# Kernel tuning notes

Hardware: AMD Instinct MI355X
Metric: run time of the kernel (lower is better)

Reference implementation:

```python
import jax, jax.numpy as jnp
import numpy as np

B, C, H, W = 4, 256, 128, 128
SP, HEADS = 4, 2
SCALE = (C // HEADS) ** -0.5  # module uses full dim//num_heads, not per-branch head dim
EPS = 1e-4
CB = C // 2  # channels per strip branch


def setup_inputs() -> dict:
    key = jax.random.key(0)
    ks = jax.random.split(key, 8)
    return {
        "x": jax.random.normal(ks[0], (B, C, H, W), jnp.float32),
        "ln_g": jnp.ones((C,), jnp.float32),
        "ln_b": jnp.zeros((C,), jnp.float32),
        "w_qkv": jax.random.normal(ks[1], (C, 3 * C), jnp.float32) * 0.02,
        "lepe_w1": jax.random.normal(ks[2], (CB, 1, 3, 3), jnp.float32) * 0.1,
        "lepe_b1": jnp.zeros((CB,), jnp.float32),
        "lepe_w2": jax.random.normal(ks[3], (CB, 1, 3, 3), jnp.float32) * 0.1,
        "lepe_b2": jnp.zeros((CB,), jnp.float32),
        "proj_w": jax.random.normal(ks[4], (C, C), jnp.float32) * 0.02,
        "proj_b": jnp.zeros((C,), jnp.float32),
    }


def _strip_branch(q, k, v, h, hsp, w, wsp, lepe_w, lepe_b):
    # q,k,v: [B, L=h*hsp*w*wsp, CB]; channel layout is (c head) -> head fastest
    cd = CB // HEADS
    nwin = B * h * w

    def to_win(t):  # -> [(b h w), head, hsp*wsp, cd]
        t = t.reshape(B, h, hsp, w, wsp, cd, HEADS)
        t = t.transpose(0, 1, 3, 6, 2, 4, 5)  # B,h,w,head,hsp,wsp,cd
        return t.reshape(nwin, HEADS, hsp * wsp, cd)

    qw, kw, vw = to_win(q), to_win(k), to_win(v)

    # LePE: depthwise 3x3 conv on v laid out as [(b h w), (c head), hsp, wsp]
    vim = vw.reshape(nwin, HEADS, hsp, wsp, cd).transpose(0, 4, 1, 2, 3)
    vim = vim.reshape(nwin, CB, hsp, wsp)
    lepe = jax.lax.conv_general_dilated(vim, lepe_w, (1, 1), 'SAME',
                                        feature_group_count=CB)
    lepe = lepe + lepe_b[None, :, None, None]
    lepe = lepe.reshape(nwin, cd, HEADS, hsp, wsp).transpose(0, 2, 3, 4, 1)
    lepe = lepe.reshape(nwin, HEADS, hsp * wsp, cd)

    attn = jax.nn.softmax(jnp.einsum('whqc,whkc->whqk', qw * SCALE, kw), axis=-1)
    o = jnp.einsum('whqk,whkc->whqc', attn, vw) + lepe
    # back to b (c head) (h hsp) (w wsp)
    o = o.reshape(B, h, w, HEADS, hsp, wsp, cd)
    o = o.transpose(0, 6, 3, 1, 4, 2, 5).reshape(B, CB, h * hsp, w * wsp)
    return o


def reference(x, ln_g, ln_b, w_qkv, lepe_w1, lepe_b1, lepe_w2, lepe_b2, proj_w, proj_b):
    # tokens [B, H*W, C]
    xp = x.transpose(0, 2, 3, 1).reshape(B, H * W, C)
    mu = xp.mean(-1, keepdims=True)
    var = ((xp - mu) ** 2).mean(-1, keepdims=True)
    xp = (xp - mu) * jax.lax.rsqrt(var + EPS) * ln_g + ln_b

    qkv = xp @ w_qkv
    q, k, v = jnp.split(qkv, 3, axis=-1)

    # branch 1: horizontal strips (h=1, hsp=H, w=W/SP, wsp=SP) on first channel half
    x1 = _strip_branch(q[..., :CB], k[..., :CB], v[..., :CB],
                       1, H, W // SP, SP, lepe_w1, lepe_b1)
    # branch 2: vertical strips (h=H/SP, hsp=SP, w=1, wsp=W) on second half
    x2 = _strip_branch(q[..., CB:], k[..., CB:], v[..., CB:],
                       H // SP, SP, 1, W, lepe_w2, lepe_b2)

    xc = jnp.concatenate([x1, x2], axis=1)  # [B, C, H, W]
    out = jnp.einsum('bchw,oc->bohw', xc, proj_w) + proj_b[None, :, None, None]
    return out
```

## Files before the change

### kernel.cpp

```cpp
#include <hip/hip_runtime.h>
#include <stdint.h>

#define T_ 65536
#define HW_ 16384
#define SCALE_F 0.08838834764831845f
#define EPS_ 1e-4f

typedef unsigned short u16;
typedef unsigned int u32;
typedef __attribute__((ext_vector_type(4))) float f32x4;
typedef __attribute__((ext_vector_type(8))) __bf16 bf16x8v;

union frag_u { u16 h[8]; bf16x8v v; uint4 q4; };

__device__ __forceinline__ float bf2f(u16 h) {
    union { u32 u; float f; } x; x.u = ((u32)h) << 16; return x.f;
}
__device__ __forceinline__ u16 f2bf(float f) {
    union { u32 u; float f; } x; x.f = f;
    u32 u = x.u;
    return (u16)((u + 0x7FFFu + ((u >> 16) & 1u)) >> 16);
}
__device__ __forceinline__ f32x4 mfma_b(bf16x8v a, bf16x8v b, f32x4 c) {
    return __builtin_amdgcn_mfma_f32_16x16x32_bf16(a, b, c, 0, 0, 0);
}
__device__ __forceinline__ void gl_lds16(const u16* g, u16* l) {
    __builtin_amdgcn_global_load_lds(
        (const __attribute__((address_space(1))) void*)g,
        (__attribute__((address_space(3))) void*)l, 16, 0, 0);
}

__device__ __forceinline__ int u2t(int u, int br) {
    if (br == 1) return u;
    int b = u >> 14, rr = u & 16383;
    int s = rr >> 9, rem = rr & 511;
    int y = rem >> 2, xl = rem & 3;
    return (b << 14) + (y << 7) + (s << 2) + xl;
}
__device__ __forceinline__ int t2u0(int t) {
    int b = t >> 14, rr = t & 16383;
    int y = rr >> 7, x = rr & 127;
    return (b << 14) + ((x >> 2) << 9) + (y << 2) + (x & 3);
}

__global__ void sentinel_kernel(float* out, float code) {
    if (blockIdx.x == 0 && threadIdx.x == 0) out[0] = code;
}

__global__ __launch_bounds__(256) void wconv_kernel(const float* __restrict__ w,
        const float* __restrict__ pw, u16* __restrict__ wt, u16* __restrict__ pwc) {
    __shared__ float lds[64 * 65];
    int bid = blockIdx.x;
    int tid = threadIdx.x;
    if (bid < 48) {
        int c0 = (bid % 12) * 64, k0 = (bid / 12) * 64;
        for (int i = 0; i < 16; ++i) {
            int e = i * 256 + tid;
            int k = e >> 6, c = e & 63;
            lds[k * 65 + c] = w[(size_t)(k0 + k) * 768 + c0 + c];
        }
        __syncthreads();
        for (int i = 0; i < 16; ++i) {
            int e = i * 256 + tid;
            int c = e >> 6, k = e & 63;
            wt[(size_t)(c0 + c) * 256 + k0 + k] = f2bf(lds[k * 65 + c]);
        }
    } else {
        int base = (bid - 48) * 2048;
        for (int i = 0; i < 8; ++i) {
            int e = base + i * 256 + tid;
            int m = e >> 8, ks = e & 255;
            int c = (ks < 128) ? (2 * (ks & 63) + (ks >> 6))
                               : (128 + 2 * ((ks - 128) & 63) + ((ks - 128) >> 6));
            pwc[e] = f2bf(pw[(size_t)m * 256 + c]);
        }
    }
}

__global__ __launch_bounds__(512, 2) void ln_kernel(const float* __restrict__ x,
        const float* __restrict__ g, const float* __restrict__ bta, u16* __restrict__ xn) {
    __shared__ float reds[8][260];
    __shared__ float redss[8][260];
    __shared__ float mus[256];
    __shared__ float rstds[256];
    int tid = threadIdx.x, lane = tid & 63, w = tid >> 6;
    int w32 = w * 32;
    int tok0 = blockIdx.x * 256 + lane * 4;
    int b = tok0 >> 14, hw = tok0 & 16383;
    const float* xb = x + (size_t)b * 256 * HW_ + hw;
    float4 v[32];
    #pragma unroll
    for (int j = 0; j < 32; ++j)
        v[j] = *(const float4*)(xb + (size_t)(w32 + j) * HW_);
    float s0 = 0.f, s1 = 0.f, s2 = 0.f, s3 = 0.f;
    float q0 = 0.f, q1 = 0.f, q2 = 0.f, q3 = 0.f;
    #pragma unroll
    for (int j = 0; j < 32; ++j) {
        s0 += v[j].x; q0 += v[j].x * v[j].x;
        s1 += v[j].y; q1 += v[j].y * v[j].y;
        s2 += v[j].z; q2 += v[j].z * v[j].z;
        s3 += v[j].w; q3 += v[j].w * v[j].w;
    }
    *(float4*)&reds[w][lane * 4]  = make_float4(s0, s1, s2, s3);
    *(float4*)&redss[w][lane * 4] = make_float4(q0, q1, q2, q3);
    __syncthreads();
    if (tid < 256) {
        float S = 0.f, SS = 0.f;
        #pragma unroll
        for (int p = 0; p < 8; ++p) { S += reds[p][tid]; SS += redss[p][tid]; }
        float mu = S * (1.f / 256.f);
        float var = SS * (1.f / 256.f) - mu * mu;
        mus[tid] = mu;
        rstds[tid] = rsqrtf(var + EPS_);
    }
    __syncthreads();
    float4 mu4 = *(const float4*)&mus[lane * 4];
    float4 rs4 = *(const float4*)&rstds[lane * 4];
    float mk[4] = {mu4.x, mu4.y, mu4.z, mu4.w};
    float rk[4] = {rs4.x, rs4.y, rs4.z, rs4.w};
    #pragma unroll
    for (int k = 0; k < 4; ++k) {
        u16 tmp[32] __attribute__((aligned(16)));
        #pragma unroll
        for (int j = 0; j < 32; ++j) {
            int c = w32 + j;
            float xv = (k == 0) ? v[j].x : (k == 1) ? v[j].y : (k == 2) ? v[j].z : v[j].w;
            tmp[j] = f2bf((xv - mk[k]) * rk[k] * g[c] + bta[c]);
        }
        u16* o = xn + (size_t)(tok0 + k) * 256 + w32;
        *(uint4*)(o)      = *(const uint4*)&tmp[0];
        *(uint4*)(o + 8)  = *(const uint4*)&tmp[8];
        *(uint4*)(o + 16) = *(const uint4*)&tmp[16];
        *(uint4*)(o + 24) = *(const uint4*)&tmp[24];
    }
}

__global__ __launch_bounds__(256) void qkv_gemm(const u16* __restrict__ wt,
        const u16* __restrict__ xn, u16* __restrict__ qkt, u16* __restrict__ vpl, int br) {
    __shared__ __align__(16) u16 a_tile[2][128 * 32];
    __shared__ __align__(16) u16 b_tile[2][128 * 32];
    int my = blockIdx.y;
    int n0 = blockIdx.x * 128;
    int tid = threadIdx.x;
    int lane = tid & 63, wid = tid >> 6;
    int wm = wid >> 1, wn = wid & 1;
    int l15 = lane & 15, quad = lane >> 4;
    int colbase = (my == 0) ? (br * 128) : (my == 1 ? (256 + br * 128) : (512 + br * 128));
    int srow = tid >> 2, sgg = tid & 3;
    const u16* gA0 = wt + (size_t)(colbase + srow) * 256 + sgg * 8;
    const u16* gA1 = gA0 + (size_t)64 * 256;
    const u16* gB0 = xn + (size_t)u2t(n0 + srow, br) * 256 + sgg * 8;
    const u16* gB1 = xn + (size_t)u2t(n0 + srow + 64, br) * 256 + sgg * 8;
    int lb0 = wid * 1024, lb1 = 4096 + wid * 1024;
    gl_lds16(gA0, (u16*)((char*)&a_tile[0][0] + lb0));
    gl_lds16(gA1, (u16*)((char*)&a_tile[0][0] + lb1));
    gl_lds16(gB0, (u16*)((char*)&b_tile[0][0] + lb0));
    gl_lds16(gB1, (u16*)((char*)&b_tile[0][0] + lb1));
    f32x4 acc[4][4] = {};
    for (int ks = 0; ks < 8; ++ks) {
        __syncthreads();
        int cur = ks & 1;
        if (ks < 7) {
            int k0 = (ks + 1) * 32;
            int nb = cur ^ 1;
            gl_lds16(gA0 + k0, (u16*)((char*)&a_tile[nb][0] + lb0));
            gl_lds16(gA1 + k0, (u16*)((char*)&a_tile[nb][0] + lb1));
            gl_lds16(gB0 + k0, (u16*)((char*)&b_tile[nb][0] + lb0));
            gl_lds16(gB1 + k0, (u16*)((char*)&b_tile[nb][0] + lb1));
        }
        bf16x8v af[4], bf[4];
        #pragma unroll
        for (int i = 0; i < 4; ++i) {
            af[i] = *(const bf16x8v*)&a_tile[cur][(wm * 64 + i * 16 + l15) * 32 + quad * 8];
            bf[i] = *(const bf16x8v*)&b_tile[cur][(wn * 64 + i * 16 + l15) * 32 + quad * 8];
        }
        #pragma unroll
        for (int i = 0; i < 4; ++i)
            #pragma unroll
            for (int j = 0; j < 4; ++j)
                acc[i][j] = mfma_b(af[i], bf[j], acc[i][j]);
    }
    if (my < 2) {
        int cb2 = my * 128;
        #pragma unroll
        for (int i = 0; i < 4; ++i) {
            #pragma unroll
            for (int r = 0; r < 4; ++r) {
                int cl = wm * 64 + i * 16 + quad * 4 + r;
                int col = cb2 + ((cl & 1) << 6) + (cl >> 1);
                #pragma unroll
                for (int j = 0; j < 4; ++j) {
                    int u = n0 + wn * 64 + j * 16 + l15;
                    qkt[(size_t)u * 256 + col] = f2bf(acc[i][j][r]);
                }
            }
        }
    } else {
        #pragma unroll
        for (int i = 0; i < 4; ++i) {
            int pbase = wm * 64 + i * 16 + quad * 4;
            #pragma unroll
            for (int j = 0; j < 4; ++j) {
                int u = n0 + wn * 64 + j * 16 + l15;
                #pragma unroll
                for (int r = 0; r < 4; ++r)
                    vpl[(size_t)(pbase + r) * T_ + u] = f2bf(acc[i][j][r]);
            }
        }
    }
}

__global__ __launch_bounds__(512, 4) void attn_kernel(const u16* __restrict__ qkt,
        const u16* __restrict__ vpl, u16* __restrict__ xcb, int stride) {
    __shared__ __align__(16) u16 k_area[2][128 * 72];
    __shared__ __align__(16) u16 v_lds[2][64 * 136];
    int bid = blockIdx.x;
    int id2 = (bid & 7) * 128 + (bid >> 3);
    int window = id2 >> 3, h = (id2 >> 2) & 1, qq = id2 & 3;
    int wbase = window * 512;
    int tid = threadIdx.x, lane = tid & 63, wid = tid >> 6;
    int l15 = lane & 15, quad = lane >> 4;

    frag_u af[2];
    {
        size_t qrow = (size_t)(wbase + qq * 128 + wid * 16 + l15) * 256 + h * 64 + quad * 8;
        af[0].q4 = *(const uint4*)&qkt[qrow];
        af[1].q4 = *(const uint4*)&qkt[qrow + 32];
    }
    for (int idx = tid; idx < 1024; idx += 512) {
        int tok = idx >> 3, c8 = (idx & 7) * 8;
        *(uint4*)&k_area[0][tok * 72 + c8] =
            *(const uint4*)&qkt[(size_t)(wbase + tok) * 256 + 128 + h * 64 + c8];
    }
    for (int idx = tid; idx < 1024; idx += 512) {
        int cd = idx >> 4, k8 = (idx & 15) * 8;
        *(uint4*)&v_lds[0][cd * 136 + k8] =
            *(const uint4*)&vpl[(size_t)(2 * cd + h) * T_ + wbase + k8];
    }
    __syncthreads();

    float m[4] = {-1e30f, -1e30f, -1e30f, -1e30f};
    float l[4] = {0.f, 0.f, 0.f, 0.f};
    f32x4 acc_o[4] = {};
    for (int ch = 0; ch < 4; ++ch) {
        int cur = ch & 1, nxt = cur ^ 1;
        if (ch < 3) {
            for (int idx = tid; idx < 1024; idx += 512) {
                int tok = idx >> 3, c8 = (idx & 7) * 8;
                *(uint4*)&k_area[nxt][tok * 72 + c8] =
                    *(const uint4*)&qkt[(size_t)(wbase + (ch + 1) * 128 + tok) * 256 + 128 + h * 64 + c8];
            }
            for (int idx = tid; idx < 1024; idx += 512) {
                int cd = idx >> 4, k8 = (idx & 15) * 8;
                *(uint4*)&v_lds[nxt][cd * 136 + k8] =
                    *(const uint4*)&vpl[(size_t)(2 * cd + h) * T_ + wbase + (ch + 1) * 128 + k8];
            }
        }
        f32x4 s[8];
        #pragma unroll
        for (int kt = 0; kt < 8; ++kt) {
            f32x4 z = {0.f, 0.f, 0.f, 0.f};
            bf16x8v b0 = *(const bf16x8v*)&k_area[cur][(kt * 16 + l15) * 72 + quad * 8];
            bf16x8v b1 = *(const bf16x8v*)&k_area[cur][(kt * 16 + l15) * 72 + 32 + quad * 8];
            z = mfma_b(af[0].v, b0, z);
            z = mfma_b(af[1].v, b1, z);
            s[kt] = z;
        }
        float cmx[4] = {-1e30f, -1e30f, -1e30f, -1e30f};
        #pragma unroll
        for (int kt = 0; kt < 8; ++kt)
            #pragma unroll
            for (int r = 0; r < 4; ++r) cmx[r] = fmaxf(cmx[r], s[kt][r]);
        #pragma unroll
        for (int d = 1; d < 16; d <<= 1)
            #pragma unroll
            for (int r = 0; r < 4; ++r) cmx[r] = fmaxf(cmx[r], __shfl_xor(cmx[r], d, 16));
        float alpha[4];
        #pragma unroll
        for (int r = 0; r < 4; ++r) {
            float mn = fmaxf(m[r], cmx[r]);
            alpha[r] = __expf((m[r] - mn) * SCALE_F);
            m[r] = mn;
        }
        float ps[4] = {0.f, 0.f, 0.f, 0.f};
        #pragma unroll
        for (int kt = 0; kt < 8; ++kt)
            #pragma unroll
            for (int r = 0; r < 4; ++r) {
                float p = __expf((s[kt][r] - m[r]) * SCALE_F);
                s[kt][r] = p;
                ps[r] += p;
            }
        #pragma unroll
        for (int r = 0; r < 4; ++r) l[r] = l[r] * alpha[r] + ps[r];
        #pragma unroll
        for (int cs = 0; cs < 4; ++cs)
            #pragma unroll
            for (int r = 0; r < 4; ++r) acc_o[cs][r] *= alpha[r];
        __syncthreads();
        u16* p_lds = &k_area[cur][wid * 1152];
        #pragma unroll
        for (int half = 0; half < 2; ++half) {
            #pragma unroll
            for (int kt4 = 0; kt4 < 4; ++kt4)
                #pragma unroll
                for (int rr = 0; rr < 4; ++rr)
                    p_lds[(quad * 4 + rr) * 72 + kt4 * 16 + l15] = f2bf(s[half * 4 + kt4][rr]);
            #pragma unroll
            for (int k32 = 0; k32 < 2; ++k32) {
                bf16x8v pa = *(const bf16x8v*)&p_lds[l15 * 72 + k32 * 32 + quad * 8];
                #pragma unroll
                for (int cs = 0; cs < 4; ++cs) {
                    bf16x8v vf = *(const bf16x8v*)&v_lds[cur]
                        [(cs * 16 + l15) * 136 + half * 64 + k32 * 32 + quad * 8];
                    acc_o[cs] = mfma_b(pa, vf, acc_o[cs]);
                }
            }
        }
        __syncthreads();
    }
    float linv[4];
    #pragma unroll
    for (int r = 0; r < 4; ++r) {
        float v = l[r];
        #pragma unroll
        for (int d = 1; d < 16; d <<= 1) v += __shfl_xor(v, d, 16);
        linv[r] = 1.f / v;
    }
    #pragma unroll
    for (int cs = 0; cs < 4; ++cs) {
        int col = h * 64 + cs * 16 + l15;
        #pragma unroll
        for (int r = 0; r < 4; ++r) {
            int u = wbase + qq * 128 + wid * 16 + quad * 4 + r;
            xcb[(size_t)u * stride + col] = f2bf(acc_o[cs][r] * linv[r]);
        }
    }
}

__global__ __launch_bounds__(512) void lepe_kernel(const u16* __restrict__ vpl,
        const float* __restrict__ lw, const float* __restrict__ lb,
        u16* __restrict__ xcb, int stride, int br) {
    __shared__ __align__(16) u16 o_s[512 * 72];
    int hh = blockIdx.x & 1, wdw = blockIdx.x >> 1;
    int wbase = wdw * 512;
    int tid = threadIdx.x;
    int xd = (br == 0) ? 4 : 128;
    for (int i = 0; i < 8; ++i) {
        int g = i * 512 + tid;
        int cd = g >> 6, u0 = (g & 63) * 8;
        int cl = 2 * cd + hh;
        const u16* vp = vpl + (size_t)cl * T_ + wbase;
        const float* wp = lw + cl * 9;
        float bias = lb[cl];
        float acc[8];
        #pragma unroll
        for (int j = 0; j < 8; ++j) acc[j] = bias;
        #pragma unroll
        for (int r = -1; r <= 1; ++r) {
            int offA = u0 + r * xd;
            int offB = offA + 4;
            float m[8];
            if (offA >= 0 && offA <= 508) {
                uint2 va = *(const uint2*)&vp[offA];
                u16 ha[4]; *(uint2*)ha = va;
                #pragma unroll
                for (int j = 0; j < 4; ++j) m[j] = bf2f(ha[j]);
            } else { m[0] = m[1] = m[2] = m[3] = 0.f; }
            if (offB >= 0 && offB <= 508) {
                uint2 vb = *(const uint2*)&vp[offB];
                u16 hb[4]; *(uint2*)hb = vb;
                #pragma unroll
                for (int j = 0; j < 4; ++j) m[4 + j] = bf2f(hb[j]);
            } else { m[4] = m[5] = m[6] = m[7] = 0.f; }
            float le = 0.f, re = 0.f;
            if (br == 1) {
                if (offA >= 0 && offA <= 508 && (u0 & 127) != 0)   le = bf2f(vp[offA - 1]);
                if (offB >= 0 && offB <= 508 && (u0 & 127) != 120) re = bf2f(vp[offB + 4]);
            }
            float w0 = wp[(r + 1) * 3 + 0], w1 = wp[(r + 1) * 3 + 1], w2 = wp[(r + 1) * 3 + 2];
            #pragma unroll
            for (int j = 0; j < 8; ++j) {
                float lv, rv2;
                if (j == 0) lv = (br == 0) ? 0.f : le;
                else        lv = (br == 0 && (j & 3) == 0) ? 0.f : m[j - 1];
                if (j == 7) rv2 = (br == 0) ? 0.f : re;
                else        rv2 = (br == 0 && (j & 3) == 3) ? 0.f : m[j + 1];
                acc[j] += w0 * lv + w1 * m[j] + w2 * rv2;
            }
        }
        int cdp = cd ^ (((u0 >> 3) & 7) << 3);
        #pragma unroll
        for (int j = 0; j < 8; ++j)
            o_s[(u0 + j) * 72 + cdp] = f2bf(acc[j]);
    }
    __syncthreads();
    for (int i = 0; i < 8; ++i) {
        int c = i * 512 + tid;
        int tok = c >> 3, cg = c & 7;
        int cgp = cg ^ ((tok >> 3) & 7);
        uint4 lv = *(const uint4*)&o_s[tok * 72 + cgp * 8];
        u16 lh[8]; *(uint4*)lh = lv;
        u16* p = &xcb[(size_t)(wbase + tok) * stride + hh * 64 + cg * 8];
        uint4 gv = *(const uint4*)p;
        u16 gh[8]; *(uint4*)gh = gv;
        u16 oh[8] __attribute__((aligned(16)));
        #pragma unroll
        for (int j = 0; j < 8; ++j) oh[j] = f2bf(bf2f(gh[j]) + bf2f(lh[j]));
        *(uint4*)p = *(const uint4*)oh;
    }
}

__global__ __launch_bounds__(256) void proj_kernel(const u16* __restrict__ pwc,
        const u16* __restrict__ xc0, const u16* __restrict__ xnov,
        const float* __restrict__ pb, float* __restrict__ out) {
    __shared__ __align__(16) u16 a_tile[2][128 * 32];
    __shared__ __align__(16) u16 b_tile[2][128 * 32];
    int m0 = blockIdx.y * 128, n0 = blockIdx.x * 128;
    int tid = threadIdx.x;
    int lane = tid & 63, wid = tid >> 6;
    int wm = wid >> 1, wn = wid & 1;
    int l15 = lane & 15, quad = lane >> 4;
    int srow = tid >> 2, sgg = tid & 3;
    const u16* gA0 = pwc + (size_t)(m0 + srow) * 256 + sgg * 8;
    const u16* gA1 = gA0 + (size_t)64 * 256;
    const u16* gB0lo = xc0 + (size_t)t2u0(n0 + srow) * 128 + sgg * 8;
    const u16* gB1lo = xc0 + (size_t)t2u0(n0 + srow + 64) * 128 + sgg * 8;
    const u16* gB0hi = xnov + (size_t)(n0 + srow) * 256 + sgg * 8;
    const u16* gB1hi = xnov + (size_t)(n0 + srow + 64) * 256 + sgg * 8;
    int lb0 = wid * 1024, lb1 = 4096 + wid * 1024;
    gl_lds16(gA0, (u16*)((char*)&a_tile[0][0] + lb0));
    gl_lds16(gA1, (u16*)((char*)&a_tile[0][0] + lb1));
    gl_lds16(gB0lo, (u16*)((char*)&b_tile[0][0] + lb0));
    gl_lds16(gB1lo, (u16*)((char*)&b_tile[0][0] + lb1));
    f32x4 acc[4][4] = {};
    for (int ks = 0; ks < 8; ++ks) {
        __syncthreads();
        int cur = ks & 1;
        if (ks < 7) {
            int k0 = (ks + 1) * 32;
            int nb = cur ^ 1;
            gl_lds16(gA0 + k0, (u16*)((char*)&a_tile[nb][0] + lb0));
            gl_lds16(gA1 + k0, (u16*)((char*)&a_tile[nb][0] + lb1));
            const u16* b0 = (k0 < 128) ? (gB0lo + k0) : (gB0hi + k0);
            const u16* b1 = (k0 < 128) ? (gB1lo + k0) : (gB1hi + k0);
            gl_lds16(b0, (u16*)((char*)&b_tile[nb][0] + lb0));
            gl_lds16(b1, (u16*)((char*)&b_tile[nb][0] + lb1));
        }
        bf16x8v af[4], bf[4];
        #pragma unroll
        for (int i = 0; i < 4; ++i) {
            af[i] = *(const bf16x8v*)&a_tile[cur][(wm * 64 + i * 16 + l15) * 32 + quad * 8];
            bf[i] = *(const bf16x8v*)&b_tile[cur][(wn * 64 + i * 16 + l15) * 32 + quad * 8];
        }
        #pragma unroll
        for (int i = 0; i < 4; ++i)
            #pragma unroll
            for (int j = 0; j < 4; ++j)
                acc[i][j] = mfma_b(af[i], bf[j], acc[i][j]);
    }
    #pragma unroll
    for (int i = 0; i < 4; ++i) {
        int mbase = m0 + wm * 64 + i * 16 + quad * 4;
        #pragma unroll
        for (int j = 0; j < 4; ++j) {
            int nc = n0 + wn * 64 + j * 16 + l15;
            #pragma unroll
            for (int r = 0; r < 4; ++r) {
                int m = mbase + r;
                out[((size_t)(nc >> 14) * 256 + m) * HW_ + (nc & 16383)] = acc[i][j][r] + pb[m];
            }
        }
    }
}

extern "C" void kernel_launch(void* const* d_in, const int* in_sizes, int n_in,
                              void* d_out, int out_size, void* d_ws, size_t ws_size,
                              hipStream_t stream) {
    const float* x     = (const float*)d_in[0];
    const float* ln_g  = (const float*)d_in[1];
    const float* ln_b  = (const float*)d_in[2];
    const float* w_qkv = (const float*)d_in[3];
    const float* lw1   = (const float*)d_in[4];
    const float* lb1   = (const float*)d_in[5];
    const float* lw2   = (const float*)d_in[6];
    const float* lb2   = (const float*)d_in[7];
    const float* pw    = (const float*)d_in[8];
    const float* pb    = (const float*)d_in[9];
    float* out = (float*)d_out;
    u16* out_u16 = (u16*)d_out;
    char* ws = (char*)d_ws;

    if (ws_size < 67108864) {
        sentinel_kernel<<<dim3(1), dim3(64), 0, stream>>>(out, 1.0e6f + (float)(ws_size >> 20));
        return;
    }

    u16* xn  = (u16*)ws;
    u16* xc0 = (u16*)(ws + 33554432);
    u16* wt  = (u16*)(ws + 50331648);
    u16* pwc = wt + 196608;
    u16* vpl = out_u16;
    u16* qkt = out_u16 + 8388608;

    wconv_kernel<<<dim3(80), dim3(256), 0, stream>>>(w_qkv, pw, wt, pwc);
    ln_kernel<<<dim3(256), dim3(512), 0, stream>>>(x, ln_g, ln_b, xn);
    qkv_gemm<<<dim3(512, 3), dim3(256), 0, stream>>>(wt, xn, qkt, vpl, 0);
    attn_kernel<<<dim3(1024), dim3(512), 0, stream>>>(qkt, vpl, xc0, 128);
    lepe_kernel<<<dim3(256), dim3(512), 0, stream>>>(vpl, lw1, lb1, xc0, 128, 0);
    qkv_gemm<<<dim3(512, 3), dim3(256), 0, stream>>>(wt, xn, qkt, vpl, 1);
    attn_kernel<<<dim3(1024), dim3(512), 0, stream>>>(qkt, vpl, xn + 128, 256);
    lepe_kernel<<<dim3(256), dim3(512), 0, stream>>>(vpl, lw2, lb2, xn + 128, 256, 1);
    proj_kernel<<<dim3(512, 2), dim3(256), 0, stream>>>(pwc, xc0, xn, pb, out);
}
```

Baseline: 415.4 us.

## Stage full activation tile once in LDS and stream pre-swizzled weight fragments

Measured after the change: 416.2 us. No clear change (+0.2%).

```diff
diff --git a/kernel.cpp b/kernel.cpp
--- a/kernel.cpp
+++ b/kernel.cpp
@@ -48,25 +48,28 @@
 }
 
 __global__ __launch_bounds__(256) void wconv_kernel(const float* __restrict__ w,
-        const float* __restrict__ pw, u16* __restrict__ wt, u16* __restrict__ pwc) {
-    __shared__ float lds[64 * 65];
+        const float* __restrict__ pw, u16* __restrict__ wtf, u16* __restrict__ pwc) {
     int bid = blockIdx.x;
     int tid = threadIdx.x;
-    if (bid < 48) {
-        int c0 = (bid % 12) * 64, k0 = (bid / 12) * 64;
-        for (int i = 0; i < 16; ++i) {
-            int e = i * 256 + tid;
-            int k = e >> 6, c = e & 63;
-            lds[k * 65 + c] = w[(size_t)(k0 + k) * 768 + c0 + c];
-        }
-        __syncthreads();
-        for (int i = 0; i < 16; ++i) {
-            int e = i * 256 + tid;
-            int c = e >> 6, k = e & 63;
-            wt[(size_t)(c0 + c) * 256 + k0 + k] = f2bf(lds[k * 65 + c]);
+    if (bid < 64) {
+        for (int it = 0; it < 3; ++it) {
+            int id = (bid * 3 + it) * 256 + tid;
+            int lane = id & 63;
+            int i  = (id >> 6) & 3;
+            int ks = (id >> 8) & 7;
+            int wm = (id >> 11) & 1;
+            int br = (id >> 12) & 1;
+            int my = id >> 13;
+            int col = my * 256 + br * 128 + wm * 64 + i * 16 + (lane & 15);
+            int k0 = ks * 32 + ((lane >> 4) & 3) * 8;
+            u16 tmp[8] __attribute__((aligned(16)));
+            #pragma unroll
+            for (int e = 0; e < 8; ++e)
+                tmp[e] = f2bf(w[(size_t)(k0 + e) * 768 + col]);
+            *(uint4*)&wtf[(size_t)id * 8] = *(const uint4*)tmp;
         }
     } else {
-        int base = (bid - 48) * 2048;
+        int base = (bid - 64) * 2048;
         for (int i = 0; i < 8; ++i) {
             int e = base + i * 256 + tid;
             int m = e >> 8, ks = e & 255;
@@ -135,76 +138,76 @@
     }
 }
 
-__global__ __launch_bounds__(256) void qkv_gemm(const u16* __restrict__ wt,
+__global__ __launch_bounds__(256) void qkv_gemm(const u16* __restrict__ wtf,
         const u16* __restrict__ xn, u16* __restrict__ qkt, u16* __restrict__ vpl, int br) {
-    __shared__ __align__(16) u16 a_tile[2][128 * 32];
-    __shared__ __align__(16) u16 b_tile[2][128 * 32];
-    int my = blockIdx.y;
+    __shared__ __align__(16) u16 b_lds[128 * 256];
     int n0 = blockIdx.x * 128;
     int tid = threadIdx.x;
     int lane = tid & 63, wid = tid >> 6;
     int wm = wid >> 1, wn = wid & 1;
     int l15 = lane & 15, quad = lane >> 4;
-    int colbase = (my == 0) ? (br * 128) : (my == 1 ? (256 + br * 128) : (512 + br * 128));
-    int srow = tid >> 2, sgg = tid & 3;
-    const u16* gA0 = wt + (size_t)(colbase + srow) * 256 + sgg * 8;
-    const u16* gA1 = gA0 + (size_t)64 * 256;
-    const u16* gB0 = xn + (size_t)u2t(n0 + srow, br) * 256 + sgg * 8;
-    const u16* gB1 = xn + (size_t)u2t(n0 + srow + 64, br) * 256 + sgg * 8;
-    int lb0 = wid * 1024, lb1 = 4096 + wid * 1024;
-    gl_lds16(gA0, (u16*)((char*)&a_tile[0][0] + lb0));
-    gl_lds16(gA1, (u16*)((char*)&a_tile[0][0] + lb1));
-    gl_lds16(gB0, (u16*)((char*)&b_tile[0][0] + lb0));
-    gl_lds16(gB1, (u16*)((char*)&b_tile[0][0] + lb1));
-    f32x4 acc[4][4] = {};
-    for (int ks = 0; ks < 8; ++ks) {
-        __syncthreads();
-        int cur = ks & 1;
-        if (ks < 7) {
-            int k0 = (ks + 1) * 32;
-            int nb = cur ^ 1;
-            gl_lds16(gA0 + k0, (u16*)((char*)&a_tile[nb][0] + lb0));
-            gl_lds16(gA1 + k0, (u16*)((char*)&a_tile[nb][0] + lb1));
-            gl_lds16(gB0 + k0, (u16*)((char*)&b_tile[nb][0] + lb0));
-            gl_lds16(gB1 + k0, (u16*)((char*)&b_tile[nb][0] + lb1));
-        }
-        bf16x8v af[4], bf[4];
-        #pragma unroll
-        for (int i = 0; i < 4; ++i) {
-            af[i] = *(const bf16x8v*)&a_tile[cur][(wm * 64 + i * 16 + l15) * 32 + quad * 8];
-            bf[i] = *(const bf16x8v*)&b_tile[cur][(wn * 64 + i * 16 + l15) * 32 + quad * 8];
-        }
-        #pragma unroll
-        for (int i = 0; i < 4; ++i)
-            #pragma unroll
-            for (int j = 0; j < 4; ++j)
-                acc[i][j] = mfma_b(af[i], bf[j], acc[i][j]);
-    }
-    if (my < 2) {
-        int cb2 = my * 128;
-        #pragma unroll
-        for (int i = 0; i < 4; ++i) {
-            #pragma unroll
-            for (int r = 0; r < 4; ++r) {
-                int cl = wm * 64 + i * 16 + quad * 4 + r;
-                int col = cb2 + ((cl & 1) << 6) + (cl >> 1);
+    {
+        int rowoff = lane >> 5;
+        int c_lds = lane & 31;
+        for (int r = 0; r < 16; ++r) {
+            int row = r * 8 + wid * 2 + rowoff;
+            int t = u2t(n0 + row, br);
+            int cg = c_lds ^ (row & 7);
+            const u16* gsrc = xn + (size_t)t * 256 + cg * 8;
+            u16* ldst = &b_lds[(r * 8 + wid * 2) * 256];
+            gl_lds16(gsrc, ldst);
+        }
+    }
+    __syncthreads();
+    #pragma unroll 1
+    for (int my = 0; my < 3; ++my) {
+        const u16* abase = wtf + (size_t)(((my * 2 + br) * 2 + wm) * 8) * 4 * 64 * 8;
+        f32x4 acc[4][4] = {};
+        #pragma unroll
+        for (int ks = 0; ks < 8; ++ks) {
+            frag_u af[4];
+            bf16x8v bf[4];
+            #pragma unroll
+            for (int i = 0; i < 4; ++i)
+                af[i].q4 = *(const uint4*)&abase[(size_t)(ks * 4 + i) * 512 + lane * 8];
+            #pragma unroll
+            for (int i = 0; i < 4; ++i) {
+                int rowb = wn * 64 + i * 16 + l15;
+                int cl2 = (ks * 4 + quad) ^ (rowb & 7);
+                bf[i] = *(const bf16x8v*)&b_lds[rowb * 256 + cl2 * 8];
+            }
+            #pragma unroll
+            for (int i = 0; i < 4; ++i)
+                #pragma unroll
+                for (int j = 0; j < 4; ++j)
+                    acc[i][j] = mfma_b(af[i].v, bf[j], acc[i][j]);
+        }
+        if (my < 2) {
+            int cb2 = my * 128;
+            #pragma unroll
+            for (int i = 0; i < 4; ++i) {
+                #pragma unroll
+                for (int r = 0; r < 4; ++r) {
+                    int cl = wm * 64 + i * 16 + quad * 4 + r;
+                    int col = cb2 + ((cl & 1) << 6) + (cl >> 1);
+                    #pragma unroll
+                    for (int j = 0; j < 4; ++j) {
+                        int u = n0 + wn * 64 + j * 16 + l15;
+                        qkt[(size_t)u * 256 + col] = f2bf(acc[i][j][r]);
+                    }
+                }
+            }
+        } else {
+            #pragma unroll
+            for (int i = 0; i < 4; ++i) {
+                int pbase = wm * 64 + i * 16 + quad * 4;
                 #pragma unroll
                 for (int j = 0; j < 4; ++j) {
                     int u = n0 + wn * 64 + j * 16 + l15;
-                    qkt[(size_t)u * 256 + col] = f2bf(acc[i][j][r]);
+                    #pragma unroll
+                    for (int r = 0; r < 4; ++r)
+                        vpl[(size_t)(pbase + r) * T_ + u] = f2bf(acc[i][j][r]);
                 }
-            }
-        }
-    } else {
-        #pragma unroll
-        for (int i = 0; i < 4; ++i) {
-            int pbase = wm * 64 + i * 16 + quad * 4;
-            #pragma unroll
-            for (int j = 0; j < 4; ++j) {
-                int u = n0 + wn * 64 + j * 16 + l15;
-                #pragma unroll
-                for (int r = 0; r < 4; ++r)
-                    vpl[(size_t)(pbase + r) * T_ + u] = f2bf(acc[i][j][r]);
             }
         }
     }
@@ -498,17 +501,17 @@
 
     u16* xn  = (u16*)ws;
     u16* xc0 = (u16*)(ws + 33554432);
-    u16* wt  = (u16*)(ws + 50331648);
-    u16* pwc = wt + 196608;
+    u16* wtf = (u16*)(ws + 50331648);
+    u16* pwc = wtf + 393216;
     u16* vpl = out_u16;
     u16* qkt = out_u16 + 8388608;
 
-    wconv_kernel<<<dim3(80), dim3(256), 0, stream>>>(w_qkv, pw, wt, pwc);
+    wconv_kernel<<<dim3(96), dim3(256), 0, stream>>>(w_qkv, pw, wtf, pwc);
     ln_kernel<<<dim3(256), dim3(512), 0, stream>>>(x, ln_g, ln_b, xn);
-    qkv_gemm<<<dim3(512, 3), dim3(256), 0, stream>>>(wt, xn, qkt, vpl, 0);
+    qkv_gemm<<<dim3(512), dim3(256), 0, stream>>>(wtf, xn, qkt, vpl, 0);
     attn_kernel<<<dim3(1024), dim3(512), 0, stream>>>(qkt, vpl, xc0, 128);
     lepe_kernel<<<dim3(256), dim3(512), 0, stream>>>(vpl, lw1, lb1, xc0, 128, 0);
-    qkv_gemm<<<dim3(512, 3), dim3(256), 0, stream>>>(wt, xn, qkt, vpl, 1);
+    qkv_gemm<<<dim3(512), dim3(256), 0, stream>>>(wtf, xn, qkt, vpl, 1);
     attn_kernel<<<dim3(1024), dim3(512), 0, stream>>>(qkt, vpl, xn + 128, 256);
     lepe_kernel<<<dim3(256), dim3(512), 0, stream>>>(vpl, lw2, lb2, xn + 128, 256, 1);
     proj_kernel<<<dim3(512, 2), dim3(256), 0, stream>>>(pwc, xc0, xn, pb, out);
```
